# Optimization experiments

Measured on AMD Instinct MI355X. Metric: run time of the kernel, lower is better.

Reference implementation:

```python
import jax, jax.numpy as jnp
import numpy as np

IN_FEATURES = 4096
OUT_FEATURES = 11008
GROUP_SIZE = 128
GROUP_COUNT = 32


def _unpack_int4_first_dim(packed):
    # packed: [rows, cols] int32; each int32 holds 8 nibbles along dim 0
    shifts = jnp.arange(0, 32, 4, dtype=jnp.int32)  # [8]
    u = (packed[:, None, :] >> shifts[None, :, None]) & 15  # [rows, 8, cols]
    return u.reshape(packed.shape[0] * 8, packed.shape[1])


def _unpack_int4_last_dim(packed):
    shifts = jnp.arange(0, 32, 4, dtype=jnp.int32)  # [8]
    u = (packed[..., None] >> shifts) & 15  # [..., cols, 8]
    return u.reshape(*packed.shape[:-1], packed.shape[-1] * 8)


def setup_inputs() -> dict:
    key = jax.random.key(0)
    k1, k2, k3, k4 = jax.random.split(key, 4)
    x = jax.random.normal(k1, (4, 2048, IN_FEATURES), dtype=jnp.float32)
    qweight = jax.random.randint(k2, (IN_FEATURES // 8, OUT_FEATURES), 0, 2147483647, dtype=jnp.int32)
    qzeros = jax.random.randint(k3, (GROUP_COUNT, OUT_FEATURES // 8), 0, 2147483647, dtype=jnp.int32)
    # small positive per-group scales, as a real GPTQ checkpoint would have
    scales = (jax.random.uniform(k4, (GROUP_COUNT, OUT_FEATURES), dtype=jnp.float32) * 0.02 + 0.001).astype(jnp.float16)
    return {"x": x, "qweight": qweight, "qzeros": qzeros, "scales": scales}


def reference(x, qweight, qzeros, scales):
    # --- dequantize (fp32, as in _dequantize_autoround) ---
    weight_int = _unpack_int4_first_dim(qweight)[:IN_FEATURES, :OUT_FEATURES]  # [IN, OUT] int32
    s = scales.astype(jnp.float32)  # [G, OUT]
    group_ids = jnp.clip(jnp.arange(IN_FEATURES) // GROUP_SIZE, 0, GROUP_COUNT - 1)  # [IN]
    zeros = _unpack_int4_last_dim(qzeros)[:GROUP_COUNT, :OUT_FEATURES].astype(jnp.float32)  # [G, OUT]
    dequant = (weight_int.astype(jnp.float32) - zeros[group_ids]) * s[group_ids]  # [IN, OUT]
    # --- F.linear in compute_dtype fp16, cast back to x.dtype ---
    w16 = dequant.astype(jnp.float16)
    out = jnp.matmul(x.astype(jnp.float16), w16)  # [B, S, OUT]
    return out.astype(x.dtype)
```

## Files before the change

kernel.cpp:

```cpp
#include <hip/hip_runtime.h>
#include <hip/hip_fp16.h>


#define M_TOT 8192
#define N_TOT 11008
#define K_TOT 4096

typedef _Float16 half2v __attribute__((ext_vector_type(2)));
typedef _Float16 half8 __attribute__((ext_vector_type(8)));
typedef float float4v __attribute__((ext_vector_type(4)));

__global__ __launch_bounds__(256) void cvt_x_fp16(const float* __restrict__ x,
                                                  _Float16* __restrict__ a16) {
    const size_t i = ((size_t)blockIdx.x * 256 + threadIdx.x) * 8;
    float4v v0 = *(const float4v*)(x + i);
    float4v v1 = *(const float4v*)(x + i + 4);
    half8 h;
    h[0] = (_Float16)v0[0]; h[1] = (_Float16)v0[1];
    h[2] = (_Float16)v0[2]; h[3] = (_Float16)v0[3];
    h[4] = (_Float16)v1[0]; h[5] = (_Float16)v1[1];
    h[6] = (_Float16)v1[2]; h[7] = (_Float16)v1[3];
    *(half8*)(a16 + i) = h;
}

__global__ __launch_bounds__(256) void dequant_w(const int* __restrict__ qw,
                                                 const unsigned* __restrict__ qz,
                                                 const float* __restrict__ sc,
                                                 _Float16* __restrict__ wt) {
    const int tid = threadIdx.x;
    const int n = blockIdx.x * 32 + (tid >> 3);
    const int r = blockIdx.y * 8 + (tid & 7);
    const int g = r >> 4;
    const _Float16 s_h = (_Float16)sc[g * N_TOT + n];
    half2v sp; sp[0] = s_h; sp[1] = s_h;
    const unsigned zraw = qz[g * (N_TOT / 8) + (n >> 3)];
    const unsigned zn = (zraw >> ((n & 7) * 4)) & 15u;
    const half2v zp = __builtin_bit_cast(half2v, 0x64006400u | zn | (zn << 16));
    const unsigned raw = (unsigned)qw[(size_t)r * N_TOT + n];
    half8 w;
    #pragma unroll
    for (int p = 0; p < 4; ++p) {
        const unsigned bits = ((raw >> (4 * p)) & 0x000F000Fu) | 0x64006400u;
        half2v d = (__builtin_bit_cast(half2v, bits) - zp) * sp;
        w[p]     = d[0];
        w[p + 4] = d[1];
    }
    *(half8*)(wt + (size_t)n * K_TOT + r * 8) = w;
}

#define BM 128
#define BN 128
#define BK 64
#define NBN (N_TOT / BN)
#define NBM (M_TOT / BM)
#define NWG (NBN * NBM)

__global__ __launch_bounds__(256) void gemm_f16(const _Float16* __restrict__ A,
                                                const _Float16* __restrict__ B,
                                                float* __restrict__ out) {
    __shared__ _Float16 As[BM * BK];
    __shared__ _Float16 Bs[BN * BK];

    const int tid = threadIdx.x;

    const int flat = blockIdx.x;
    const int swz = (flat & 7) * (NWG / 8) + (flat >> 3);
    const int n0 = (swz % NBN) * BN;
    const int m0 = (swz / NBN) * BM;

    const int wave = tid >> 6;
    const int lane = tid & 63;
    const int wr = wave >> 1;
    const int wc = wave & 1;
    const int l16 = lane & 15;
    const int quad = lane >> 4;

    const int srow = wave * 8 + (lane >> 3);
    const int scol = ((lane & 7) ^ (lane >> 3)) * 8;

    const int ksw = (l16 & 7) * 8;

    float4v acc[4][4] = {};

    for (int k0 = 0; k0 < K_TOT; k0 += BK) {
        __syncthreads();
        #pragma unroll
        for (int i = 0; i < 4; ++i) {
            const _Float16* ga = A + (size_t)(m0 + i * 32 + srow) * K_TOT + k0 + scol;
            __builtin_amdgcn_global_load_lds(
                (const __attribute__((address_space(1))) void*)ga,
                (__attribute__((address_space(3))) void*)&As[(i * 32 + wave * 8) * BK],
                16, 0, 0);
            const _Float16* gb = B + (size_t)(n0 + i * 32 + srow) * K_TOT + k0 + scol;
            __builtin_amdgcn_global_load_lds(
                (const __attribute__((address_space(1))) void*)gb,
                (__attribute__((address_space(3))) void*)&Bs[(i * 32 + wave * 8) * BK],
                16, 0, 0);
        }
        __syncthreads();

        #pragma unroll
        for (int kk = 0; kk < 2; ++kk) {
            half8 af[4], bf[4];
            #pragma unroll
            for (int i = 0; i < 4; ++i)
                af[i] = *(const half8*)&As[(wr * 64 + i * 16 + l16) * BK
                                           + ((kk * 32 + quad * 8) ^ ksw)];
            #pragma unroll
            for (int j = 0; j < 4; ++j)
                bf[j] = *(const half8*)&Bs[(wc * 64 + j * 16 + l16) * BK
                                           + ((kk * 32 + quad * 8) ^ ksw)];
            #pragma unroll
            for (int i = 0; i < 4; ++i)
                #pragma unroll
                for (int j = 0; j < 4; ++j)
                    acc[i][j] = __builtin_amdgcn_mfma_f32_16x16x32_f16(af[i], bf[j], acc[i][j], 0, 0, 0);
        }
    }

    float* o = out + (size_t)(m0 + wr * 64) * N_TOT + (n0 + wc * 64);
    #pragma unroll
    for (int i = 0; i < 4; ++i)
        #pragma unroll
        for (int j = 0; j < 4; ++j)
            #pragma unroll
            for (int r = 0; r < 4; ++r)
                __builtin_nontemporal_store(acc[i][j][r],
                    &o[(size_t)(i * 16 + quad * 4 + r) * N_TOT + (j * 16 + l16)]);
}

#define LDK 72

__global__ __launch_bounds__(256) void gptq_fused_gemm(
    const float* __restrict__ x,
    const int* __restrict__ qw,
    const unsigned* __restrict__ qz,
    const float* __restrict__ sc,
    float* __restrict__ out)
{
    __shared__ _Float16 As[BM * LDK];
    __shared__ _Float16 Bs[BN * LDK];

    const int tid = threadIdx.x;
    const int m0 = blockIdx.y * BM;
    const int n0 = blockIdx.x * BN;

    const int wave = tid >> 6;
    const int lane = tid & 63;
    const int wr = wave >> 1;
    const int wc = wave & 1;
    const int l16 = lane & 15;
    const int quad = lane >> 4;

    const int a_k8 = tid & 7;
    const int a_m  = tid >> 3;
    const int b_n  = tid & 127;
    const int b_rr = tid >> 7;
    const int ncol = n0 + b_n;

    float4v acc[4][4] = {};

    for (int k0 = 0; k0 < K_TOT; k0 += BK) {
        __syncthreads();
        {
            const float* src = x + (size_t)(m0 + a_m) * K_TOT + k0 + a_k8 * 8;
            #pragma unroll
            for (int i = 0; i < 4; ++i) {
                const float* p = src + (size_t)(i * 32) * K_TOT;
                float4v v0 = *(const float4v*)p;
                float4v v1 = *(const float4v*)(p + 4);
                half8 h;
                h[0] = (_Float16)v0[0]; h[1] = (_Float16)v1[0];
                h[2] = (_Float16)v0[1]; h[3] = (_Float16)v1[1];
                h[4] = (_Float16)v0[2]; h[5] = (_Float16)v1[2];
                h[6] = (_Float16)v0[3]; h[7] = (_Float16)v1[3];
                *(half8*)&As[(a_m + 32 * i) * LDK + a_k8 * 8] = h;
            }
        }
        {
            const int g = k0 >> 7;
            const _Float16 s_h = (_Float16)sc[g * N_TOT + ncol];
            half2v sp; sp[0] = s_h; sp[1] = s_h;
            const unsigned zraw = qz[g * (N_TOT / 8) + (ncol >> 3)];
            const unsigned zn = (zraw >> ((ncol & 7) * 4)) & 15u;
            const half2v zp = __builtin_bit_cast(half2v, 0x64006400u | zn | (zn << 16));
            const int krow0 = k0 >> 3;
            #pragma unroll
            for (int i = 0; i < 4; ++i) {
                const int rr = b_rr + 2 * i;
                const unsigned raw = (unsigned)qw[(size_t)(krow0 + rr) * N_TOT + ncol];
                half8 w;
                #pragma unroll
                for (int p = 0; p < 4; ++p) {
                    const unsigned bits = ((raw >> (4 * p)) & 0x000F000Fu) | 0x64006400u;
                    half2v d = (__builtin_bit_cast(half2v, bits) - zp) * sp;
                    w[2 * p]     = d[0];
                    w[2 * p + 1] = d[1];
                }
                *(half8*)&Bs[b_n * LDK + rr * 8] = w;
            }
        }
        __syncthreads();
        #pragma unroll
        for (int kk = 0; kk < 2; ++kk) {
            half8 af[4], bf[4];
            #pragma unroll
            for (int i = 0; i < 4; ++i)
                af[i] = *(const half8*)&As[(wr * 64 + i * 16 + l16) * LDK + kk * 32 + quad * 8];
            #pragma unroll
            for (int j = 0; j < 4; ++j)
                bf[j] = *(const half8*)&Bs[(wc * 64 + j * 16 + l16) * LDK + kk * 32 + quad * 8];
            #pragma unroll
            for (int i = 0; i < 4; ++i)
                #pragma unroll
                for (int j = 0; j < 4; ++j)
                    acc[i][j] = __builtin_amdgcn_mfma_f32_16x16x32_f16(af[i], bf[j], acc[i][j], 0, 0, 0);
        }
    }

    float* o = out + (size_t)(m0 + wr * 64) * N_TOT + (n0 + wc * 64);
    #pragma unroll
    for (int i = 0; i < 4; ++i)
        #pragma unroll
        for (int j = 0; j < 4; ++j)
            #pragma unroll
            for (int r = 0; r < 4; ++r)
                o[(size_t)(i * 16 + quad * 4 + r) * N_TOT + (j * 16 + l16)] = acc[i][j][r];
}

extern "C" void kernel_launch(void* const* d_in, const int* in_sizes, int n_in,
                              void* d_out, int out_size, void* d_ws, size_t ws_size,
                              hipStream_t stream) {
    const float* x = (const float*)d_in[0];
    const int* qw = (const int*)d_in[1];
    const unsigned* qz = (const unsigned*)d_in[2];
    const float* sc = (const float*)d_in[3];
    float* out = (float*)d_out;

    const size_t a16_bytes = (size_t)M_TOT * K_TOT * 2;
    const size_t wt_bytes  = (size_t)N_TOT * K_TOT * 2;

    if (ws_size >= a16_bytes + wt_bytes) {
        _Float16* A16 = (_Float16*)d_ws;
        _Float16* Wt  = (_Float16*)((char*)d_ws + a16_bytes);
        cvt_x_fp16<<<dim3((M_TOT * K_TOT) / (256 * 8)), dim3(256), 0, stream>>>(x, A16);
        dequant_w<<<dim3(N_TOT / 32, 512 / 8), dim3(256), 0, stream>>>(qw, qz, sc, Wt);
        gemm_f16<<<dim3(NWG), dim3(256), 0, stream>>>(A16, Wt, out);
    } else {
        gptq_fused_gemm<<<dim3(N_TOT / BN, M_TOT / BM), dim3(256), 0, stream>>>(x, qw, qz, sc, out);
    }
}
```

Measured before the change: 1.481 ms.

## Replace fp16 GEMM with 256x256 eight-wave kernel using 4-stage async LDS pipeline

Replaces the single-buffered 128x128 GEMM with a 256x256 tile kernel using 8 waves per block and a K-step of 32. A 4-deep ring of LDS buffers is filled with direct global-to-LDS loads, and explicit vmcnt waits and barriers interleave the next tiles' loads with MFMA bursts. s_setprio is raised around the MFMA bursts. The larger tile raises data reuse per LDS byte and hides global latency, at the cost of about 128KB of LDS per block (one block per CU), more register pressure, and hand-counted waitcnt logic that must stay correct.

New measurement: 1.225 ms. -17.3%, faster.

```diff
diff --git a/kernel.cpp b/kernel.cpp
--- a/kernel.cpp
+++ b/kernel.cpp
@@ -48,87 +48,138 @@
     *(half8*)(wt + (size_t)n * K_TOT + r * 8) = w;
 }
 
+#define TBM 256
+#define TBN 256
+#define TBK 32
+#define NKT (K_TOT / TBK)
+#define TNBN (N_TOT / TBN)
+#define TNBM (M_TOT / TBM)
+#define TNWG (TNBN * TNBM)
+
+__global__ __launch_bounds__(512, 2) void gemm_f16_8p(const _Float16* __restrict__ A,
+                                                      const _Float16* __restrict__ B,
+                                                      float* __restrict__ out) {
+    __shared__ _Float16 As[4 * 256 * 32];
+    __shared__ _Float16 Bs[4 * 256 * 32];
+
+    const int tid = threadIdx.x;
+    const int wave = tid >> 6;
+    const int lane = tid & 63;
+
+    const int flat = blockIdx.x;
+    const int swz = (flat & 7) * (TNWG / 8) + (flat >> 3);
+    const int n0 = (swz % TNBN) * TBN;
+    const int m0 = (swz / TNBN) * TBM;
+
+    const int wm = wave >> 2;
+    const int wn = wave & 3;
+    const int l16 = lane & 15;
+    const int quad = lane >> 4;
+
+    const int s_row  = wave * 16 + (lane >> 2);
+    const int s_slot = ((lane & 3) ^ ((lane >> 2) & 3)) * 8;
+    const _Float16* a_src = A + (size_t)(m0 + s_row) * K_TOT + s_slot;
+    const _Float16* b_src = B + (size_t)(n0 + s_row) * K_TOT + s_slot;
+    const int s_dst = wave * 512;
+
+    const int rd_off = (quad ^ (l16 & 3)) * 8;
+
+    #define STAGE_A(t) do {                                                      \
+        const int b_ = (t) & 3;                                                  \
+        const _Float16* s0_ = a_src + (size_t)(t) * TBK;                         \
+        __builtin_amdgcn_global_load_lds(                                        \
+            (const __attribute__((address_space(1))) void*)s0_,                  \
+            (__attribute__((address_space(3))) void*)&As[b_ * 8192 + s_dst],     \
+            16, 0, 0);                                                           \
+        __builtin_amdgcn_global_load_lds(                                        \
+            (const __attribute__((address_space(1))) void*)(s0_ + (size_t)128 * K_TOT), \
+            (__attribute__((address_space(3))) void*)&As[b_ * 8192 + 4096 + s_dst],     \
+            16, 0, 0);                                                           \
+    } while (0)
+
+    #define STAGE_B(t) do {                                                      \
+        const int b_ = (t) & 3;                                                  \
+        const _Float16* s0_ = b_src + (size_t)(t) * TBK;                         \
+        __builtin_amdgcn_global_load_lds(                                        \
+            (const __attribute__((address_space(1))) void*)s0_,                  \
+            (__attribute__((address_space(3))) void*)&Bs[b_ * 8192 + s_dst],     \
+            16, 0, 0);                                                           \
+        __builtin_amdgcn_global_load_lds(                                        \
+            (const __attribute__((address_space(1))) void*)(s0_ + (size_t)128 * K_TOT), \
+            (__attribute__((address_space(3))) void*)&Bs[b_ * 8192 + 4096 + s_dst],     \
+            16, 0, 0);                                                           \
+    } while (0)
+
+    float4v acc[8][4] = {};
+
+    STAGE_A(0); STAGE_B(0);
+    STAGE_A(1); STAGE_B(1);
+    STAGE_A(2); STAGE_B(2);
+    asm volatile("s_waitcnt vmcnt(8)" ::: "memory");
+    __builtin_amdgcn_s_barrier();
+
+    #define STEP(s, DO_STAGE, WAIT_STMT) do {                                    \
+        const int b = (s) & 3;                                                   \
+        const _Float16* Ab = &As[b * 8192];                                      \
+        const _Float16* Bb = &Bs[b * 8192];                                      \
+        half8 af[4], bf[4];                                                      \
+                            \
+        _Pragma("unroll")                                                        \
+        for (int i = 0; i < 4; ++i)                                              \
+            af[i] = *(const half8*)&Ab[(wm * 128 + i * 16 + l16) * TBK + rd_off];\
+        _Pragma("unroll")                                                        \
+        for (int j = 0; j < 4; ++j)                                              \
+            bf[j] = *(const half8*)&Bb[(wn * 64 + j * 16 + l16) * TBK + rd_off]; \
+        if (DO_STAGE) STAGE_A((s) + 3);                                          \
+        __builtin_amdgcn_s_barrier();                                            \
+        __builtin_amdgcn_s_setprio(1);                                           \
+        _Pragma("unroll")                                                        \
+        for (int i = 0; i < 4; ++i)                                              \
+            _Pragma("unroll")                                                    \
+            for (int j = 0; j < 4; ++j)                                          \
+                acc[i][j] = __builtin_amdgcn_mfma_f32_16x16x32_f16(af[i], bf[j], acc[i][j], 0, 0, 0); \
+        __builtin_amdgcn_s_setprio(0);                                           \
+        __builtin_amdgcn_s_barrier();                                            \
+                                     \
+        _Pragma("unroll")                                                        \
+        for (int i = 0; i < 4; ++i)                                              \
+            af[i] = *(const half8*)&Ab[(wm * 128 + 64 + i * 16 + l16) * TBK + rd_off]; \
+        if (DO_STAGE) STAGE_B((s) + 3);                                          \
+        __builtin_amdgcn_s_barrier();                                            \
+        __builtin_amdgcn_s_setprio(1);                                           \
+        _Pragma("unroll")                                                        \
+        for (int i = 0; i < 4; ++i)                                              \
+            _Pragma("unroll")                                                    \
+            for (int j = 0; j < 4; ++j)                                          \
+                acc[4 + i][j] = __builtin_amdgcn_mfma_f32_16x16x32_f16(af[i], bf[j], acc[4 + i][j], 0, 0, 0); \
+        __builtin_amdgcn_s_setprio(0);                                           \
+        WAIT_STMT;                                                               \
+        __builtin_amdgcn_s_barrier();                                            \
+    } while (0)
+
+    for (int s = 0; s < NKT - 3; ++s)
+        STEP(s, 1, asm volatile("s_waitcnt vmcnt(8)" ::: "memory"));
+    STEP(NKT - 3, 0, asm volatile("s_waitcnt vmcnt(4)" ::: "memory"));
+    STEP(NKT - 2, 0, asm volatile("s_waitcnt vmcnt(0)" ::: "memory"));
+    STEP(NKT - 1, 0, (void)0);
+
+    #undef STEP
+    #undef STAGE_A
+    #undef STAGE_B
+
+    float* o = out + (size_t)(m0 + wm * 128) * N_TOT + (n0 + wn * 64);
+    #pragma unroll
+    for (int mf = 0; mf < 8; ++mf)
+        #pragma unroll
+        for (int j = 0; j < 4; ++j)
+            #pragma unroll
+            for (int r = 0; r < 4; ++r)
+                o[(size_t)(mf * 16 + quad * 4 + r) * N_TOT + (j * 16 + l16)] = acc[mf][j][r];
+}
+
 #define BM 128
 #define BN 128
 #define BK 64
-#define NBN (N_TOT / BN)
-#define NBM (M_TOT / BM)
-#define NWG (NBN * NBM)
-
-__global__ __launch_bounds__(256) void gemm_f16(const _Float16* __restrict__ A,
-                                                const _Float16* __restrict__ B,
-                                                float* __restrict__ out) {
-    __shared__ _Float16 As[BM * BK];
-    __shared__ _Float16 Bs[BN * BK];
-
-    const int tid = threadIdx.x;
-
-    const int flat = blockIdx.x;
-    const int swz = (flat & 7) * (NWG / 8) + (flat >> 3);
-    const int n0 = (swz % NBN) * BN;
-    const int m0 = (swz / NBN) * BM;
-
-    const int wave = tid >> 6;
-    const int lane = tid & 63;
-    const int wr = wave >> 1;
-    const int wc = wave & 1;
-    const int l16 = lane & 15;
-    const int quad = lane >> 4;
-
-    const int srow = wave * 8 + (lane >> 3);
-    const int scol = ((lane & 7) ^ (lane >> 3)) * 8;
-
-    const int ksw = (l16 & 7) * 8;
-
-    float4v acc[4][4] = {};
-
-    for (int k0 = 0; k0 < K_TOT; k0 += BK) {
-        __syncthreads();
-        #pragma unroll
-        for (int i = 0; i < 4; ++i) {
-            const _Float16* ga = A + (size_t)(m0 + i * 32 + srow) * K_TOT + k0 + scol;
-            __builtin_amdgcn_global_load_lds(
-                (const __attribute__((address_space(1))) void*)ga,
-                (__attribute__((address_space(3))) void*)&As[(i * 32 + wave * 8) * BK],
-                16, 0, 0);
-            const _Float16* gb = B + (size_t)(n0 + i * 32 + srow) * K_TOT + k0 + scol;
-            __builtin_amdgcn_global_load_lds(
-                (const __attribute__((address_space(1))) void*)gb,
-                (__attribute__((address_space(3))) void*)&Bs[(i * 32 + wave * 8) * BK],
-                16, 0, 0);
-        }
-        __syncthreads();
-
-        #pragma unroll
-        for (int kk = 0; kk < 2; ++kk) {
-            half8 af[4], bf[4];
-            #pragma unroll
-            for (int i = 0; i < 4; ++i)
-                af[i] = *(const half8*)&As[(wr * 64 + i * 16 + l16) * BK
-                                           + ((kk * 32 + quad * 8) ^ ksw)];
-            #pragma unroll
-            for (int j = 0; j < 4; ++j)
-                bf[j] = *(const half8*)&Bs[(wc * 64 + j * 16 + l16) * BK
-                                           + ((kk * 32 + quad * 8) ^ ksw)];
-            #pragma unroll
-            for (int i = 0; i < 4; ++i)
-                #pragma unroll
-                for (int j = 0; j < 4; ++j)
-                    acc[i][j] = __builtin_amdgcn_mfma_f32_16x16x32_f16(af[i], bf[j], acc[i][j], 0, 0, 0);
-        }
-    }
-
-    float* o = out + (size_t)(m0 + wr * 64) * N_TOT + (n0 + wc * 64);
-    #pragma unroll
-    for (int i = 0; i < 4; ++i)
-        #pragma unroll
-        for (int j = 0; j < 4; ++j)
-            #pragma unroll
-            for (int r = 0; r < 4; ++r)
-                __builtin_nontemporal_store(acc[i][j][r],
-                    &o[(size_t)(i * 16 + quad * 4 + r) * N_TOT + (j * 16 + l16)]);
-}
-
 #define LDK 72
 
 __global__ __launch_bounds__(256) void gptq_fused_gemm(
@@ -245,7 +296,7 @@
         _Float16* Wt  = (_Float16*)((char*)d_ws + a16_bytes);
         cvt_x_fp16<<<dim3((M_TOT * K_TOT) / (256 * 8)), dim3(256), 0, stream>>>(x, A16);
         dequant_w<<<dim3(N_TOT / 32, 512 / 8), dim3(256), 0, stream>>>(qw, qz, sc, Wt);
-        gemm_f16<<<dim3(NWG), dim3(256), 0, stream>>>(A16, Wt, out);
+        gemm_f16_8p<<<dim3(TNWG), dim3(512), 0, stream>>>(A16, Wt, out);
     } else {
         gptq_fused_gemm<<<dim3(N_TOT / BN, M_TOT / BM), dim3(256), 0, stream>>>(x, qw, qz, sc, out);
     }
```
